# Optimization experiments

Hardware: AMD Instinct MI355X
Metric: run time of the kernel (lower is better)

The kernel has to match this reference:

```python
import jax, jax.numpy as jnp
import numpy as np

N = 10000   # num_nodes
F = 64      # latent_dim
U = 128     # num_units
B = 8       # batch
K = 2       # gcn_step
E = 160000  # edges (avg degree 16)
M = 2 * K + 1  # num_matrices = len(supports)*gcn_step + 1


def setup_inputs() -> dict:
    rng = np.random.default_rng(0)
    rows = rng.integers(0, N, E).astype(np.int32)
    cols = rng.integers(0, N, E).astype(np.int32)
    vals = (rng.random(E).astype(np.float32) + 0.1)
    # random-walk normalization D^{-1} A, per the original utils.calculate_random_walk_matrix
    deg_out = np.zeros(N, np.float32); np.add.at(deg_out, rows, vals)
    deg_in = np.zeros(N, np.float32); np.add.at(deg_in, cols, vals)
    # support1 = (D_out^{-1} A)^T : out[c] += vals/d_out[r] * x[r]  -> dst=cols, src=rows
    w1 = vals / np.maximum(deg_out[rows], 1e-8)
    # support2 = (D_in^{-1} A^T)^T : out[r] += vals/d_in[c] * x[c]  -> dst=rows, src=cols
    w2 = vals / np.maximum(deg_in[cols], 1e-8)

    key = jax.random.key(0)
    ks = jax.random.split(key, 4)

    def xavier(k, shape):
        std = (2.0 / (shape[0] + shape[1])) ** 0.5
        return jax.random.normal(k, shape, jnp.float32) * std

    return {
        'y': jax.random.normal(ks[0], (B, N * F), jnp.float32),
        'W_lat': xavier(ks[1], (M * F, F)),
        'b_lat': jnp.ones((F,), jnp.float32),   # bias_start=1.0, shared (keyed by length)
        'W_units': xavier(ks[2], (M * F, U)),
        'b_units': jnp.zeros((U,), jnp.float32),
        'W_final': xavier(ks[3], (M * U, F)),
        'sup1_w': jnp.asarray(w1),
        'sup2_w': jnp.asarray(w2),
        'edge_rows': jnp.asarray(rows),
        'edge_cols': jnp.asarray(cols),
    }


def _spmm(dst, src, w, x):
    # sparse matmul S @ x with S given as COO edge list; x: (N, Fin, B)
    return jax.ops.segment_sum(w[:, None, None] * x[src], dst, num_segments=N)


def _gconv(x, supports, W, b):
    # x: (B, N, Fin) -> (B, N*Fout); Chebyshev diffusion convolution
    Bsz, n, fin = x.shape
    x0 = jnp.transpose(x, (1, 2, 0))  # (N, Fin, B)
    xs = [x0]
    for dst, src, w in supports:
        xk_2 = x0
        x1 = _spmm(dst, src, w, x0)
        xs.append(x1)
        for _ in range(2, K + 1):
            x2 = 2.0 * _spmm(dst, src, w, x1) - xk_2
            xs.append(x2)
            xk_2, x1 = x1, x2
    X = jnp.stack(xs, axis=-1)                       # (N, Fin, B, M)
    X = jnp.transpose(X, (2, 0, 1, 3)).reshape(Bsz * n, fin * len(xs))  # feature-major, matrix-minor
    out = X @ W + b
    return out.reshape(Bsz, n * W.shape[1])


def reference(y, W_lat, b_lat, W_units, b_units, W_final, sup1_w, sup2_w, edge_rows, edge_cols):
    supports = [(edge_cols, edge_rows, sup1_w), (edge_rows, edge_cols, sup2_w)]
    x = y.reshape(B, N, F)
    # theta gate (bias_start=1.0 via shared b_lat)
    theta = jax.nn.sigmoid(_gconv(x, supports, W_lat, b_lat))
    # ode_func_net: gen_layers=1 hidden gconv + final gconv (final bias is shared b_lat!)
    c = jnp.tanh(_gconv(x, supports, W_units, b_units)).reshape(B, N, U)
    c = jnp.tanh(_gconv(c, supports, W_final, b_lat))
    return -theta * c
```

## Files before the change

### kernel.cpp

```cpp
#include <hip/hip_runtime.h>

#define N_NODES 10000
#define NEDGE 160000
#define NB 80000
#define EPAD (NEDGE + 8 * N_NODES)

typedef unsigned int u32;
typedef unsigned short u16;
typedef __attribute__((ext_vector_type(8))) short short8;
typedef __attribute__((ext_vector_type(4))) float float4v;

__device__ __forceinline__ u16 f2bf(float f) {
    u32 u = __float_as_uint(f);
    return (u16)((u + 0x7fffu + ((u >> 16) & 1u)) >> 16);
}
__device__ __forceinline__ float lo16(u32 u) { return __uint_as_float(u << 16); }
__device__ __forceinline__ float hi16(u32 u) { return __uint_as_float(u & 0xffff0000u); }
__device__ __forceinline__ u32 pack2(float a, float b) {
    return (u32)f2bf(a) | (((u32)f2bf(b)) << 16);
}
__device__ __forceinline__ float fast_tanh(float v) {
    return 1.f - 2.f / (__expf(2.f * v) + 1.f);
}

static const size_t SLAB = (size_t)NB * 64;

__global__ __launch_bounds__(256) void prepcount_kernel(
    const float2* __restrict__ y, u32* __restrict__ X0,
    const float* __restrict__ W_lat, const float* __restrict__ W_units,
    u16* __restrict__ bpk12, const float* __restrict__ W_final, u16* __restrict__ bpkP,
    const int* __restrict__ rows, const int* __restrict__ cols, int* __restrict__ cnt) {
    int b = blockIdx.x, t = threadIdx.x;
    if (b < 10000) {
        int idx = b * 256 + t;
        int fh = idx & 31;
        int rb = idx >> 5;
        int bb = rb & 7;
        int n = rb >> 3;
        float2 v = y[((size_t)bb * N_NODES + n) * 32 + fh];
        X0[idx] = pack2(v.x, v.y);
    } else if (b < 10240) {
        int idx = (b - 10000) * 256 + t;
        int j = idx & 7;
        int lane = (idx >> 3) & 63;
        int rest = idx >> 9;
        int ct = rest % 12;
        int ks = rest / 12;
        int k = ks * 32 + (lane >> 4) * 8 + j;
        int col = ct * 16 + (lane & 15);
        int wrow = (k % 64) * 5 + (k / 64);
        float v = (col < 64) ? W_lat[wrow * 64 + col] : W_units[wrow * 128 + (col - 64)];
        bpk12[idx] = f2bf(v);
    } else if (b < 10400) {
        int idx = (b - 10240) * 256 + t;
        int j8 = idx & 7;
        int lane = (idx >> 3) & 63;
        int rest = idx >> 9;
        int ct = rest % 20;
        int ks = rest / 20;
        int k = ks * 32 + (lane >> 4) * 8 + j8;
        int col = ct * 16 + (lane & 15);
        int slot = col >> 6, j = col & 63;
        float v;
        if (slot == 0)
            v = W_final[(k * 5 + 0) * 64 + j] - W_final[(k * 5 + 2) * 64 + j] -
                W_final[(k * 5 + 4) * 64 + j];
        else
            v = W_final[(k * 5 + slot) * 64 + j];
        bpkP[idx] = f2bf(v);
    } else {
        int e = (b - 10400) * 256 + t;
        atomicAdd(&cnt[cols[e]], 1);
        atomicAdd(&cnt[N_NODES + rows[e]], 1);
    }
}

__global__ void blocksum_kernel(const int* __restrict__ cnt, int* __restrict__ bsums) {
    __shared__ int red[4];
    int arr = blockIdx.x / 40;
    int c = blockIdx.x % 40;
    int idx = c * 256 + threadIdx.x;
    int v = (idx < N_NODES) ? ((cnt[arr * N_NODES + idx] + 7) & ~7) : 0;
#pragma unroll
    for (int off = 32; off; off >>= 1) v += __shfl_down(v, off, 64);
    int wv = threadIdx.x >> 6, ln = threadIdx.x & 63;
    if (ln == 0) red[wv] = v;
    __syncthreads();
    if (threadIdx.x == 0) bsums[blockIdx.x] = red[0] + red[1] + red[2] + red[3];
}

__global__ void scanapply_kernel(int* __restrict__ cnt, const int* __restrict__ bsums,
                                 int* __restrict__ rowptr1, int* __restrict__ rowptr2) {
    __shared__ int lds[256];
    int arr = blockIdx.x / 40;
    int c = blockIdx.x % 40;
    int base = 0;
    for (int i = 0; i < c; i++) base += bsums[arr * 40 + i];
    int idx = c * 256 + threadIdx.x;
    bool ok = idx < N_NODES;
    int v = ok ? ((cnt[arr * N_NODES + idx] + 7) & ~7) : 0;
    int t = threadIdx.x;
    lds[t] = v;
    __syncthreads();
    for (int off = 1; off < 256; off <<= 1) {
        int add = (t >= off) ? lds[t - off] : 0;
        __syncthreads();
        lds[t] += add;
        __syncthreads();
    }
    int excl = lds[t] - v + base;
    if (ok) {
        int* rp = arr ? rowptr2 : rowptr1;
        rp[idx] = excl;
        cnt[arr * N_NODES + idx] = excl;
    }
    if (c == 39 && t == 255) {
        (arr ? rowptr2 : rowptr1)[N_NODES] = base + lds[255];
    }
}

__global__ void scatter_kernel(const int* __restrict__ rows, const int* __restrict__ cols,
                               const float* __restrict__ w1, const float* __restrict__ w2,
                               int* __restrict__ cur1, int* __restrict__ cur2,
                               int2* __restrict__ edges1, int2* __restrict__ edges2) {
    int e = blockIdx.x * 256 + threadIdx.x;
    if (e < NEDGE) {
        int r = rows[e], c = cols[e];
        int p1 = atomicAdd(&cur1[c], 1);
        edges1[p1] = make_int2(r, __float_as_int(w1[e]));
        int p2 = atomicAdd(&cur2[r], 1);
        edges2[p2] = make_int2(c, __float_as_int(w2[e]));
    }
}

__device__ __forceinline__ void gacc(float* acc, float w, uint4 u) {
    acc[0] += w * lo16(u.x); acc[1] += w * hi16(u.x);
    acc[2] += w * lo16(u.y); acc[3] += w * hi16(u.y);
    acc[4] += w * lo16(u.z); acc[5] += w * hi16(u.z);
    acc[6] += w * lo16(u.w); acc[7] += w * hi16(u.w);
}

__device__ __forceinline__ void gather_sliced(const u32* __restrict__ Xin,
                                              const int* __restrict__ rp,
                                              const int2* __restrict__ eg,
                                              int row, bool valid, int su, int l,
                                              float* acc) {
    int e = 0, e1 = 0;
    if (valid) {
        e = rp[row] + l;
        e1 = rp[row + 1];
    }
    while (__ballot(e < e1)) {
        int2 me = make_int2(0, 0);
        if (e < e1) me = eg[e];
#pragma unroll
        for (int j = 0; j < 8; j++) {
            int s = __shfl(me.x, j, 8);
            float w = __int_as_float(__shfl(me.y, j, 8));
            uint4 u = *(const uint4*)(Xin + (size_t)s * 256 + su + l * 4);
            gacc(acc, w, u);
        }
        e += 8;
    }
}

__global__ __launch_bounds__(256) void spmm2_kernel(
    const u32* __restrict__ XinA, const u32* __restrict__ XprevA, u32* __restrict__ XoutA,
    const u32* __restrict__ XinB, const u32* __restrict__ XprevB, u32* __restrict__ XoutB,
    const int* __restrict__ rowptr1, const int2* __restrict__ edges1,
    const int* __restrict__ rowptr2, const int2* __restrict__ edges2,
    float alpha, float beta) {
    int t = threadIdx.x;
    int lane = t & 63;
    int g = lane >> 3, l = lane & 7;
    int slice = blockIdx.x & 7;
    int chunk = blockIdx.x >> 3;
    int su = slice * 32;
    int v = chunk * 32 + (t >> 6) * 8 + g;
    bool hB = v >= N_NODES;
    int n = hB ? v - N_NODES : v;
    const u32* Xin = hB ? XinB : XinA;
    const u32* Xprev = hB ? XprevB : XprevA;
    u32* Xout = hB ? XoutB : XoutA;
    const int* rp = hB ? rowptr2 : rowptr1;
    const int2* eg = hB ? edges2 : edges1;

    float acc[8] = {0.f, 0.f, 0.f, 0.f, 0.f, 0.f, 0.f, 0.f};
    gather_sliced(Xin, rp, eg, n, true, su, l, acc);

    size_t o = (size_t)n * 256 + su + l * 4;
    if (beta != 0.f) {
        uint4 p = *(const uint4*)(Xprev + o);
        acc[0] = alpha * acc[0] + beta * lo16(p.x); acc[1] = alpha * acc[1] + beta * hi16(p.x);
        acc[2] = alpha * acc[2] + beta * lo16(p.y); acc[3] = alpha * acc[3] + beta * hi16(p.y);
        acc[4] = alpha * acc[4] + beta * lo16(p.z); acc[5] = alpha * acc[5] + beta * hi16(p.z);
        acc[6] = alpha * acc[6] + beta * lo16(p.w); acc[7] = alpha * acc[7] + beta * hi16(p.w);
    } else {
#pragma unroll
        for (int i = 0; i < 8; i++) acc[i] *= alpha;
    }
    uint4 r;
    r.x = pack2(acc[0], acc[1]);
    r.y = pack2(acc[2], acc[3]);
    r.z = pack2(acc[4], acc[5]);
    r.w = pack2(acc[6], acc[7]);
    *(uint4*)(Xout + o) = r;
}

__global__ __launch_bounds__(256) void spmm_final_kernel(
    const u32* __restrict__ T1, const u32* __restrict__ T2,
    const u32* __restrict__ Q, const u32* __restrict__ theta,
    const int* __restrict__ rowptr1, const int2* __restrict__ edges1,
    const int* __restrict__ rowptr2, const int2* __restrict__ edges2,
    float* __restrict__ outF) {
    int t = threadIdx.x;
    int lane = t & 63;
    int g = lane >> 3, l = lane & 7;
    int slice = blockIdx.x & 7;
    int chunk = blockIdx.x >> 3;
    int su = slice * 32;
    int n = chunk * 32 + (t >> 6) * 8 + g;
    bool valid = n < N_NODES;

    float acc[8] = {0.f, 0.f, 0.f, 0.f, 0.f, 0.f, 0.f, 0.f};
    gather_sliced(T1, rowptr1, edges1, n, valid, su, l, acc);
    gather_sliced(T2, rowptr2, edges2, n, valid, su, l, acc);
    if (!valid) return;

    size_t o = (size_t)n * 256 + su + l * 4;
    uint4 q = *(const uint4*)(Q + o);
    uint4 th = *(const uint4*)(theta + o);
    float res[8];
    res[0] = -lo16(th.x) * fast_tanh(lo16(q.x) + acc[0]);
    res[1] = -hi16(th.x) * fast_tanh(hi16(q.x) + acc[1]);
    res[2] = -lo16(th.y) * fast_tanh(lo16(q.y) + acc[2]);
    res[3] = -hi16(th.y) * fast_tanh(hi16(q.y) + acc[3]);
    res[4] = -lo16(th.z) * fast_tanh(lo16(q.z) + acc[4]);
    res[5] = -hi16(th.z) * fast_tanh(hi16(q.z) + acc[5]);
    res[6] = -lo16(th.w) * fast_tanh(lo16(q.w) + acc[6]);
    res[7] = -hi16(th.w) * fast_tanh(hi16(q.w) + acc[7]);
    float* dst = outF + (size_t)slice * (N_NODES * 64) + (size_t)n * 64 + l * 8;
    *(float4*)(dst) = make_float4(res[0], res[1], res[2], res[3]);
    *(float4*)(dst + 4) = make_float4(res[4], res[5], res[6], res[7]);
}

struct Slabs { const u16* p[5]; };

template <int FIN, int NM, int NOUT, int CT, int MODE>
__global__ __launch_bounds__(256, 4) void gemm_kernel(
    Slabs A, const u16* __restrict__ Bp, const float* __restrict__ bias1,
    const float* __restrict__ bias2, u16* __restrict__ O1, u16* __restrict__ O2) {
    constexpr int K = NM * FIN;
    constexpr int KS = K / 32;
    constexpr int CTT = NOUT / 16;
    static_assert(CT * 4 == CTT, "4 waves = 4 col groups");

    int t = threadIdx.x;
    int lane = t & 63;
    int wave = t >> 6;
    int ctBase = wave * CT;
    size_t rowBase = (size_t)blockIdx.x * 16;
    int mrow = lane & 15;
    int kq = lane >> 4;

    short8 a[KS];
#pragma unroll
    for (int ks = 0; ks < KS; ks++) {
        int k = ks * 32 + kq * 8;
        a[ks] = *(const short8*)(A.p[k / FIN] + (rowBase + mrow) * FIN + (k % FIN));
    }

    float4v acc[CT];
#pragma unroll
    for (int c = 0; c < CT; c++) acc[c] = (float4v){0.f, 0.f, 0.f, 0.f};

    short8 bc[CT];
#pragma unroll
    for (int ct = 0; ct < CT; ct++)
        bc[ct] = *(const short8*)(Bp + ((size_t)(ctBase + ct) * 64 + lane) * 8);
#pragma unroll
    for (int ks = 0; ks < KS; ks++) {
        short8 bn[CT];
        if (ks + 1 < KS) {
#pragma unroll
            for (int ct = 0; ct < CT; ct++)
                bn[ct] = *(const short8*)(Bp +
                          ((size_t)((ks + 1) * CTT + ctBase + ct) * 64 + lane) * 8);
        }
#pragma unroll
        for (int ct = 0; ct < CT; ct++)
            acc[ct] = __builtin_amdgcn_mfma_f32_16x16x32_bf16(bc[ct], a[ks], acc[ct], 0, 0, 0);
        if (ks + 1 < KS) {
#pragma unroll
            for (int ct = 0; ct < CT; ct++) bc[ct] = bn[ct];
        }
    }

    size_t r = rowBase + mrow;
#pragma unroll
    for (int ct = 0; ct < CT; ct++) {
        int col0 = (ctBase + ct) * 16 + kq * 4;
        float v[4];
#pragma unroll
        for (int i = 0; i < 4; i++) v[i] = acc[ct][i];
        if (MODE == 0) {
            if (col0 < 64) {
#pragma unroll
                for (int i = 0; i < 4; i++) v[i] += bias1[col0 + i];
            }
            uint2 w = make_uint2(pack2(v[0], v[1]), pack2(v[2], v[3]));
            *(uint2*)(O1 + (size_t)(col0 >> 6) * SLAB + r * 64 + (col0 & 63)) = w;
        } else {
            if (col0 < 64) {
#pragma unroll
                for (int i = 0; i < 4; i++)
                    v[i] = 1.f / (1.f + __expf(-(v[i] + bias1[col0 + i])));
                uint2 w = make_uint2(pack2(v[0], v[1]), pack2(v[2], v[3]));
                *(uint2*)(O1 + r * 64 + col0) = w;
            } else {
#pragma unroll
                for (int i = 0; i < 4; i++)
                    v[i] = fast_tanh(v[i] + bias2[col0 - 64 + i]);
                uint2 w = make_uint2(pack2(v[0], v[1]), pack2(v[2], v[3]));
                *(uint2*)(O2 + r * 128 + (col0 - 64)) = w;
            }
        }
    }
}

extern "C" void kernel_launch(void* const* d_in, const int* in_sizes, int n_in,
                              void* d_out, int out_size, void* d_ws, size_t ws_size,
                              hipStream_t stream) {
    const float2* y    = (const float2*)d_in[0];
    const float* W_lat = (const float*)d_in[1];
    const float* b_lat = (const float*)d_in[2];
    const float* W_units = (const float*)d_in[3];
    const float* b_units = (const float*)d_in[4];
    const float* W_final = (const float*)d_in[5];
    const float* sup1w = (const float*)d_in[6];
    const float* sup2w = (const float*)d_in[7];
    const int* rows    = (const int*)d_in[8];
    const int* cols    = (const int*)d_in[9];
    float* out = (float*)d_out;

    char* ws = (char*)d_ws;
    size_t off = 0;
    auto alloc = [&](size_t bytes) -> void* {
        void* p = ws + off;
        off += (bytes + 511) & ~(size_t)511;
        return p;
    };
    int* rowptr1 = (int*)alloc((N_NODES + 1) * 4);
    int* rowptr2 = (int*)alloc((N_NODES + 1) * 4);
    int* cnt = (int*)alloc((size_t)2 * N_NODES * 4);
    int* bsums = (int*)alloc(80 * 4);
    int2* edges1 = (int2*)alloc((size_t)EPAD * 8);
    int2* edges2 = (int2*)alloc((size_t)EPAD * 8);
    u16* bpk12 = (u16*)alloc((size_t)61440 * 2);
    u16* bpkP = (u16*)alloc((size_t)40960 * 2);
    u16* theta = (u16*)alloc((size_t)NB * 64 * 2);
    u16* S = (u16*)alloc((size_t)5 * NB * 64 * 2);
    u16* H0 = (u16*)alloc((size_t)NB * 128 * 2);
    u16* T1 = (u16*)alloc((size_t)NB * 64 * 2);
    u16* T2 = (u16*)alloc((size_t)NB * 64 * 2);

    hipMemsetAsync(cnt, 0, (size_t)2 * N_NODES * 4, stream);
    hipMemsetAsync(edges1, 0, (size_t)EPAD * 8, stream);
    hipMemsetAsync(edges2, 0, (size_t)EPAD * 8, stream);
    prepcount_kernel<<<11025, 256, 0, stream>>>(y, (u32*)S, W_lat, W_units, bpk12,
                                                W_final, bpkP, rows, cols, cnt);
    blocksum_kernel<<<80, 256, 0, stream>>>(cnt, bsums);
    scanapply_kernel<<<80, 256, 0, stream>>>(cnt, bsums, rowptr1, rowptr2);
    scatter_kernel<<<625, 256, 0, stream>>>(rows, cols, sup1w, sup2w,
                                            cnt, cnt + N_NODES, edges1, edges2);

    const u32* S0 = (const u32*)S;
    u32* X1 = (u32*)(S + 1 * SLAB);
    u32* X2 = (u32*)(S + 2 * SLAB);
    u32* X3 = (u32*)(S + 3 * SLAB);
    u32* X4 = (u32*)(S + 4 * SLAB);
    spmm2_kernel<<<5000, 256, 0, stream>>>(S0, nullptr, X1, S0, nullptr, X3,
                                           rowptr1, edges1, rowptr2, edges2, 1.f, 0.f);
    spmm2_kernel<<<5000, 256, 0, stream>>>(X1, S0, X2, X3, S0, X4,
                                           rowptr1, edges1, rowptr2, edges2, 2.f, -1.f);

    Slabs SX;
    for (int m = 0; m < 5; m++) SX.p[m] = S + (size_t)m * SLAB;
    gemm_kernel<64, 5, 192, 3, 1><<<5000, 256, 0, stream>>>(SX, bpk12, b_lat, b_units, theta, H0);

    Slabs SH;
    SH.p[0] = H0;
    gemm_kernel<128, 1, 320, 5, 0><<<5000, 256, 0, stream>>>(SH, bpkP, b_lat, nullptr, S, nullptr);

    const u32* Q  = (const u32*)(S + 0 * SLAB);
    const u32* P1 = (const u32*)(S + 1 * SLAB);
    const u32* P2 = (const u32*)(S + 2 * SLAB);
    const u32* P3 = (const u32*)(S + 3 * SLAB);
    const u32* P4 = (const u32*)(S + 4 * SLAB);
    spmm2_kernel<<<5000, 256, 0, stream>>>(P2, P1, (u32*)T1, P4, P3, (u32*)T2,
                                           rowptr1, edges1, rowptr2, edges2, 2.f, 1.f);
    spmm_final_kernel<<<2504, 256, 0, stream>>>((const u32*)T1, (const u32*)T2, Q,
                                                (const u32*)theta,
                                                rowptr1, edges1, rowptr2, edges2, out);
}
```

Baseline: 342.7 us.

## Fuse the two dense GEMM stages through LDS, dropping the H0 buffer

The first-layer GEMM (theta and hidden units) and the second GEMM (hidden to the five output slabs) now run in one kernel. The tanh hidden activations for each 16-row tile stay in shared memory instead of being written to and read back from a global H0 buffer. This removes a large global round-trip and one kernel launch. In exchange the kernel uses more registers and LDS, and it writes into the same S slabs it reads, which relies on each block touching only its own rows.

New measurement: 326.0 us. 4.9% less time.

```diff
diff --git a/kernel.cpp b/kernel.cpp
--- a/kernel.cpp
+++ b/kernel.cpp
@@ -246,84 +246,104 @@
 
 struct Slabs { const u16* p[5]; };
 
-template <int FIN, int NM, int NOUT, int CT, int MODE>
-__global__ __launch_bounds__(256, 4) void gemm_kernel(
-    Slabs A, const u16* __restrict__ Bp, const float* __restrict__ bias1,
-    const float* __restrict__ bias2, u16* __restrict__ O1, u16* __restrict__ O2) {
-    constexpr int K = NM * FIN;
-    constexpr int KS = K / 32;
-    constexpr int CTT = NOUT / 16;
-    static_assert(CT * 4 == CTT, "4 waves = 4 col groups");
+__global__ __launch_bounds__(256, 4) void gemm_fused_kernel(
+    Slabs A, const u16* __restrict__ Bp1, const u16* __restrict__ Bp2,
+    const float* __restrict__ b_lat, const float* __restrict__ b_units,
+    u16* __restrict__ theta, u16* __restrict__ Sout) {
+    __shared__ u16 Hlds[16][136];
 
     int t = threadIdx.x;
     int lane = t & 63;
     int wave = t >> 6;
-    int ctBase = wave * CT;
-    size_t rowBase = (size_t)blockIdx.x * 16;
     int mrow = lane & 15;
     int kq = lane >> 4;
-
-    short8 a[KS];
-#pragma unroll
-    for (int ks = 0; ks < KS; ks++) {
-        int k = ks * 32 + kq * 8;
-        a[ks] = *(const short8*)(A.p[k / FIN] + (rowBase + mrow) * FIN + (k % FIN));
-    }
-
-    float4v acc[CT];
-#pragma unroll
-    for (int c = 0; c < CT; c++) acc[c] = (float4v){0.f, 0.f, 0.f, 0.f};
-
-    short8 bc[CT];
-#pragma unroll
-    for (int ct = 0; ct < CT; ct++)
-        bc[ct] = *(const short8*)(Bp + ((size_t)(ctBase + ct) * 64 + lane) * 8);
-#pragma unroll
-    for (int ks = 0; ks < KS; ks++) {
-        short8 bn[CT];
-        if (ks + 1 < KS) {
+    size_t rowBase = (size_t)blockIdx.x * 16;
+    size_t r = rowBase + mrow;
+
+    {
+        constexpr int KS = 10, CTT = 12, CT = 3;
+        int ctBase = wave * CT;
+        float4v acc[CT];
+#pragma unroll
+        for (int c = 0; c < CT; c++) acc[c] = (float4v){0.f, 0.f, 0.f, 0.f};
+
+        short8 bc[CT];
+#pragma unroll
+        for (int ct = 0; ct < CT; ct++)
+            bc[ct] = *(const short8*)(Bp1 + ((size_t)(ctBase + ct) * 64 + lane) * 8);
+#pragma unroll
+        for (int ks = 0; ks < KS; ks++) {
+            int k = ks * 32 + kq * 8;
+            short8 a = *(const short8*)(A.p[ks / 2] + r * 64 + (k & 63));
+            short8 bn[CT];
+            if (ks + 1 < KS) {
+#pragma unroll
+                for (int ct = 0; ct < CT; ct++)
+                    bn[ct] = *(const short8*)(Bp1 +
+                              ((size_t)((ks + 1) * CTT + ctBase + ct) * 64 + lane) * 8);
+            }
 #pragma unroll
             for (int ct = 0; ct < CT; ct++)
-                bn[ct] = *(const short8*)(Bp +
-                          ((size_t)((ks + 1) * CTT + ctBase + ct) * 64 + lane) * 8);
+                acc[ct] = __builtin_amdgcn_mfma_f32_16x16x32_bf16(bc[ct], a, acc[ct], 0, 0, 0);
+            if (ks + 1 < KS) {
+#pragma unroll
+                for (int ct = 0; ct < CT; ct++) bc[ct] = bn[ct];
+            }
         }
-#pragma unroll
-        for (int ct = 0; ct < CT; ct++)
-            acc[ct] = __builtin_amdgcn_mfma_f32_16x16x32_bf16(bc[ct], a[ks], acc[ct], 0, 0, 0);
-        if (ks + 1 < KS) {
-#pragma unroll
-            for (int ct = 0; ct < CT; ct++) bc[ct] = bn[ct];
+
+#pragma unroll
+        for (int ct = 0; ct < CT; ct++) {
+            int col0 = (ctBase + ct) * 16 + kq * 4;
+            float v[4];
+#pragma unroll
+            for (int i = 0; i < 4; i++) v[i] = acc[ct][i];
+            if (col0 < 64) {
+#pragma unroll
+                for (int i = 0; i < 4; i++)
+                    v[i] = 1.f / (1.f + __expf(-(v[i] + b_lat[col0 + i])));
+                uint2 w = make_uint2(pack2(v[0], v[1]), pack2(v[2], v[3]));
+                *(uint2*)(theta + r * 64 + col0) = w;
+            } else {
+#pragma unroll
+                for (int i = 0; i < 4; i++)
+                    v[i] = fast_tanh(v[i] + b_units[col0 - 64 + i]);
+                uint2 w = make_uint2(pack2(v[0], v[1]), pack2(v[2], v[3]));
+                *(uint2*)(&Hlds[mrow][col0 - 64]) = w;
+            }
         }
     }
-
-    size_t r = rowBase + mrow;
-#pragma unroll
-    for (int ct = 0; ct < CT; ct++) {
-        int col0 = (ctBase + ct) * 16 + kq * 4;
-        float v[4];
-#pragma unroll
-        for (int i = 0; i < 4; i++) v[i] = acc[ct][i];
-        if (MODE == 0) {
-            if (col0 < 64) {
-#pragma unroll
-                for (int i = 0; i < 4; i++) v[i] += bias1[col0 + i];
+    __syncthreads();
+
+    {
+        constexpr int KS = 4, CTT = 20, CT = 5;
+        int ctBase = wave * CT;
+        float4v acc[CT];
+#pragma unroll
+        for (int c = 0; c < CT; c++) acc[c] = (float4v){0.f, 0.f, 0.f, 0.f};
+
+#pragma unroll
+        for (int ks = 0; ks < KS; ks++) {
+            int k = ks * 32 + kq * 8;
+            short8 a = *(const short8*)(&Hlds[mrow][k]);
+#pragma unroll
+            for (int ct = 0; ct < CT; ct++) {
+                short8 b = *(const short8*)(Bp2 +
+                            ((size_t)(ks * CTT + ctBase + ct) * 64 + lane) * 8);
+                acc[ct] = __builtin_amdgcn_mfma_f32_16x16x32_bf16(b, a, acc[ct], 0, 0, 0);
+            }
+        }
+
+#pragma unroll
+        for (int ct = 0; ct < CT; ct++) {
+            int col0 = (ctBase + ct) * 16 + kq * 4;
+            float v[4];
+#pragma unroll
+            for (int i = 0; i < 4; i++) {
+                v[i] = acc[ct][i];
+                if (col0 < 64) v[i] += b_lat[col0 + i];
             }
             uint2 w = make_uint2(pack2(v[0], v[1]), pack2(v[2], v[3]));
-            *(uint2*)(O1 + (size_t)(col0 >> 6) * SLAB + r * 64 + (col0 & 63)) = w;
-        } else {
-            if (col0 < 64) {
-#pragma unroll
-                for (int i = 0; i < 4; i++)
-                    v[i] = 1.f / (1.f + __expf(-(v[i] + bias1[col0 + i])));
-                uint2 w = make_uint2(pack2(v[0], v[1]), pack2(v[2], v[3]));
-                *(uint2*)(O1 + r * 64 + col0) = w;
-            } else {
-#pragma unroll
-                for (int i = 0; i < 4; i++)
-                    v[i] = fast_tanh(v[i] + bias2[col0 - 64 + i]);
-                uint2 w = make_uint2(pack2(v[0], v[1]), pack2(v[2], v[3]));
-                *(uint2*)(O2 + r * 128 + (col0 - 64)) = w;
-            }
+            *(uint2*)(Sout + (size_t)(col0 >> 6) * SLAB + r * 64 + (col0 & 63)) = w;
         }
     }
 }
@@ -360,7 +380,6 @@
     u16* bpkP = (u16*)alloc((size_t)40960 * 2);
     u16* theta = (u16*)alloc((size_t)NB * 64 * 2);
     u16* S = (u16*)alloc((size_t)5 * NB * 64 * 2);
-    u16* H0 = (u16*)alloc((size_t)NB * 128 * 2);
     u16* T1 = (u16*)alloc((size_t)NB * 64 * 2);
     u16* T2 = (u16*)alloc((size_t)NB * 64 * 2);
 
@@ -386,11 +405,8 @@
 
     Slabs SX;
     for (int m = 0; m < 5; m++) SX.p[m] = S + (size_t)m * SLAB;
-    gemm_kernel<64, 5, 192, 3, 1><<<5000, 256, 0, stream>>>(SX, bpk12, b_lat, b_units, theta, H0);
-
-    Slabs SH;
-    SH.p[0] = H0;
-    gemm_kernel<128, 1, 320, 5, 0><<<5000, 256, 0, stream>>>(SH, bpkP, b_lat, nullptr, S, nullptr);
+    gemm_fused_kernel<<<5000, 256, 0, stream>>>(SX, bpk12, bpkP, b_lat, b_units,
+                                                theta, S);
 
     const u32* Q  = (const u32*)(S + 0 * SLAB);
     const u32* P1 = (const u32*)(S + 1 * SLAB);
```
